# Kernel tuning notes

Measured on AMD Instinct MI355X. Metric: run time of the kernel, lower is better.

The kernel has to match this reference:

```python
import jax, jax.numpy as jnp
import numpy as np
from jax import lax

B, C, T = 16, 1, 2097152
DS = 16  # downsample_factor


def setup_inputs() -> dict:
    key = jax.random.key(0)
    audio = jax.random.normal(key, (B, C, T), dtype=jnp.float32) * 0.5
    sr, attack_ms, release_ms = 44100.0, 10.0, 100.0
    tc = float(np.exp(-np.log10(9.0)))  # exp(-log10(9)) time-constant numerator
    return {
        'audio': audio,
        'threshold': jnp.array([-20.0], jnp.float32),
        'ratio': jnp.array([4.0], jnp.float32),
        'makeup': jnp.array([3.0], jnp.float32),
        'attack_time': jnp.array([tc / (sr * attack_ms * 0.001 * DS)], jnp.float32),
        'release_time': jnp.array([tc / (sr * release_ms * 0.001 * DS)], jnp.float32),
    }


def _linear_downsample(x, factor):
    # F.interpolate(mode='linear', align_corners=False, scale_factor=1/factor)
    Tin = x.shape[-1]
    Tout = Tin // factor
    scale = Tin / Tout
    src = (jnp.arange(Tout, dtype=jnp.float32) + 0.5) * scale - 0.5
    src = jnp.clip(src, 0.0, Tin - 1)
    x0 = jnp.floor(src).astype(jnp.int32)
    x1 = jnp.minimum(x0 + 1, Tin - 1)
    w = src - x0.astype(jnp.float32)
    return x[..., x0] * (1.0 - w) + x[..., x1] * w


def _upsample_with_windows(x, up):
    # x: [B, C, F] framewise envelope; overlap-add with periodic Hann, hop=up
    xb = jnp.concatenate([x, x[..., -1:]], axis=-1)  # add endpoint
    n = jnp.arange(2 * up, dtype=jnp.float32)
    win = 0.5 * (1.0 - jnp.cos(2.0 * jnp.pi * n / (2 * up)))  # torch.hann_window (periodic)
    frames = xb[..., None] * win  # [B, C, F+1, 2*up]
    bsz, ch, nf, fl = frames.shape
    L = (nf - 1) * up + fl
    idx = (jnp.arange(nf)[:, None] * up + jnp.arange(fl)[None, :]).reshape(-1)
    out = jnp.zeros((bsz, ch, L), frames.dtype).at[:, :, idx].add(frames.reshape(bsz, ch, -1))
    return out[:, :, up:-up]


def reference(audio, threshold, ratio, makeup, attack_time, release_time):
    audio_db = 20.0 * jnp.log10(jnp.abs(audio) + 1e-8)
    comp_db = jnp.where(audio_db > threshold,
                        threshold + (audio_db - threshold) / ratio,
                        audio_db)
    gain = comp_db - audio_db  # [B, C, T], static gain reduction in dB (<= 0)
    gd = _linear_downsample(gain, DS)  # [B, C, T//DS]
    # sequential attack/release gain smoothing (one-pole recurrence) over frames
    gd_t = jnp.moveaxis(gd, -1, 0)  # [T//DS, B, C]
    def step(prev, tgt):
        new = jnp.where(tgt >= prev,
                        attack_time * prev + (1.0 - attack_time) * tgt,
                        release_time * prev + (1.0 - release_time) * tgt)
        return new, new
    _, ys = lax.scan(step, gd_t[0], gd_t)
    gs = jnp.moveaxis(ys, 0, -1)  # smoothed gain, [B, C, T//DS]
    gup = _upsample_with_windows(gs, DS)[..., :gain.shape[-1]]
    out_db = audio_db + gup + makeup
    out = 10.0 ** (out_db / 20.0)
    return jnp.where(audio < 0, -out, out)
```

## Files before the change

### kernel.cpp

```cpp
#include <hip/hip_runtime.h>
#include <math.h>

#define B_SZ 16
#define T_LEN 2097152
#define F_LEN (T_LEN / 16)
#define NBLOCKS 8192
#define K_LOG 0.16609640474436813f

typedef float f32x4 __attribute__((ext_vector_type(4)));

#define KEEP4(v) asm volatile("" :: "v"(v.x), "v"(v.y), "v"(v.z), "v"(v.w))
#define LGKM_FENCE() asm volatile("s_waitcnt lgkmcnt(0)" ::: "memory")

__device__ __forceinline__ float gain_db(float s, float thr, float slope) {
    float db = 6.0205999132796239f * __log2f(fabsf(s) + 1e-8f);
    float ov = db - thr;
    return ov > 0.0f ? ov * slope : 0.0f;
}
__device__ __forceinline__ float step1(float y, float t, float at, float rt) {
    return fmaf((t >= y) ? at : rt, y - t, t);
}
__device__ __forceinline__ float win_sel(int p, float a, float b, float c, float d) {
    float lo = (p & 1) ? b : a;
    float hi = (p & 1) ? d : c;
    return (p & 2) ? hi : lo;
}

__global__ __launch_bounds__(256) void k_fused(const float4* __restrict__ audio4,
                                               const float* __restrict__ thr_p,
                                               const float* __restrict__ ratio_p,
                                               const float* __restrict__ mk_p,
                                               const float* __restrict__ at_p,
                                               const float* __restrict__ rt_p,
                                               float4* __restrict__ out4) {
    __shared__ float  gd_s[4][84];
    __shared__ float2 yp_s[4][64];

    const int tid  = threadIdx.x;
    const int lane = tid & 63;
    const int wv   = tid >> 6;
    const int b    = blockIdx.x >> 9;
    const int bib  = blockIdx.x & 511;
    const int W0   = (bib << 8) + (wv << 6);

    const float*  Af = (const float*)audio4 + (size_t)b * T_LEN;
    const float4* A4 = audio4 + (size_t)b * (T_LEN / 4) + (size_t)W0 * 4;
    float4*       O4 = out4  + (size_t)b * (T_LEN / 4) + (size_t)W0 * 4;

    float4 xs0 = A4[lane];
    float4 xs1 = A4[lane + 64];
    float4 xs2 = A4[lane + 128];
    float4 xs3 = A4[lane + 192];
    KEEP4(xs0); KEEP4(xs1); KEEP4(xs2); KEEP4(xs3);

    float t7 = 0.0f, t8 = 0.0f;
    if (lane < 17) {
        int fr = (lane < 16) ? (W0 - 16 + lane) : (W0 + 64);
        fr = fr < 0 ? 0 : (fr > F_LEN - 1 ? F_LEN - 1 : fr);
        t7 = Af[(size_t)fr * 16 + 7];
        t8 = Af[(size_t)fr * 16 + 8];
    }

    const float thr   = thr_p[0];
    const float slope = 1.0f / ratio_p[0] - 1.0f;
    const float at = at_p[0], rt = rt_p[0];
    const int   p  = lane & 3;

#define GDJ(J, XV) {                                                   \
        float v  = (p == 1) ? XV.w : XV.x;                             \
        float g  = gain_db(v, thr, slope);                             \
        float gp = __shfl_xor(g, 3);                                   \
        if (p == 1) gd_s[wv][16 + 16 * J + (lane >> 2)] = 0.5f * (g + gp); }
    GDJ(0, xs0) GDJ(1, xs1) GDJ(2, xs2) GDJ(3, xs3)
#undef GDJ
    if (lane < 17) {
        float gw = 0.5f * (gain_db(t7, thr, slope) + gain_db(t8, thr, slope));
        gd_s[wv][(lane < 16) ? lane : 80] = gw;
    }
    LGKM_FENCE();

    if (lane < 4) {
        const float4* gp4 = reinterpret_cast<const float4*>(&gd_s[wv][16 * lane]);
        float4 r0 = gp4[0], r1 = gp4[1], r2 = gp4[2], r3 = gp4[3];
        float4 r4 = gp4[4], r5 = gp4[5], r6 = gp4[6], r7 = gp4[7];
        float  rE = gd_s[wv][16 * lane + 32];
        __builtin_amdgcn_sched_barrier(0);
        bool exact = (bib == 0) && (wv == 0) && (lane == 0);
        float y;
        if (exact) {
            y = r4.x;
        } else {
            y = r0.x;
            y = step1(y, r0.y, at, rt); y = step1(y, r0.z, at, rt); y = step1(y, r0.w, at, rt);
            y = step1(y, r1.x, at, rt); y = step1(y, r1.y, at, rt); y = step1(y, r1.z, at, rt); y = step1(y, r1.w, at, rt);
            y = step1(y, r2.x, at, rt); y = step1(y, r2.y, at, rt); y = step1(y, r2.z, at, rt); y = step1(y, r2.w, at, rt);
            y = step1(y, r3.x, at, rt); y = step1(y, r3.y, at, rt); y = step1(y, r3.z, at, rt); y = step1(y, r3.w, at, rt);
            y = step1(y, r4.x, at, rt);
        }
        float2* ypb = &yp_s[wv][16 * lane];
        float yn;
#define PAIRSTEP(T, IDX) yn = step1(y, T, at, rt); ypb[IDX] = make_float2(y, yn); y = yn;
        PAIRSTEP(r4.y, 0)  PAIRSTEP(r4.z, 1)  PAIRSTEP(r4.w, 2)
        PAIRSTEP(r5.x, 3)  PAIRSTEP(r5.y, 4)  PAIRSTEP(r5.z, 5)  PAIRSTEP(r5.w, 6)
        PAIRSTEP(r6.x, 7)  PAIRSTEP(r6.y, 8)  PAIRSTEP(r6.z, 9)  PAIRSTEP(r6.w, 10)
        PAIRSTEP(r7.x, 11) PAIRSTEP(r7.y, 12) PAIRSTEP(r7.z, 13) PAIRSTEP(r7.w, 14)
        PAIRSTEP(rE, 15)
#undef PAIRSTEP
    }
    LGKM_FENCE();

    const float mkK = mk_p[0] * K_LOG;
    const int fsub = lane >> 2;
    const float wl0 = win_sel(p, 0.0f,                 0.14644660940672624f, 0.5f,                 0.85355339059327376f);
    const float wl1 = win_sel(p, 0.00960735979838478f, 0.22221488349019889f, 0.59754516100806413f, 0.91573480615127262f);
    const float wl2 = win_sel(p, 0.03806023374435663f, 0.30865828381745511f, 0.69134171618254489f, 0.96193976625564337f);
    const float wl3 = win_sel(p, 0.08426519384872738f, 0.40245483899193587f, 0.77778511650980111f, 0.99039264020161522f);

#define OUTC(C, WL) { float m = fabsf(C) + 1e-8f;                                   \
        float vv = m * __builtin_amdgcn_exp2f(fmaf(fmaf(dd, WL, gq), K_LOG, mkK));  \
        C = (C < 0.0f) ? -vv : vv; }
#define OUTJ(J, XV) {                                                               \
        float2 pr = yp_s[wv][16 * J + fsub];                                        \
        float gq = pr.x;                                                            \
        float dd = (W0 + 16 * J + fsub == F_LEN - 1) ? 0.0f : (pr.y - pr.x);        \
        OUTC(XV.x, wl0) OUTC(XV.y, wl1) OUTC(XV.z, wl2) OUTC(XV.w, wl3)             \
        O4[64 * J + lane] = XV; }
    OUTJ(0, xs0) OUTJ(1, xs1) OUTJ(2, xs2) OUTJ(3, xs3)
#undef OUTJ
#undef OUTC
}

extern "C" void kernel_launch(void* const* d_in, const int* in_sizes, int n_in,
                              void* d_out, int out_size, void* d_ws, size_t ws_size,
                              hipStream_t stream) {
    const float* audio  = (const float*)d_in[0];
    const float* thr    = (const float*)d_in[1];
    const float* ratio  = (const float*)d_in[2];
    const float* makeup = (const float*)d_in[3];
    const float* at     = (const float*)d_in[4];
    const float* rt     = (const float*)d_in[5];

    k_fused<<<NBLOCKS, 256, 0, stream>>>((const float4*)audio, thr, ratio, makeup,
                                         at, rt, (float4*)d_out);
}
```

Baseline: 237.9 us.

## Process four tiles per wave with double-buffered register prefetch

Each wave now handles four consecutive 64-frame tiles instead of one, and the grid shrinks to a quarter of the blocks. The next tile's audio is loaded into a second register set while the current tile is processed. The warm-up window gains are reused from the previous tile's tail held in shared memory, which removes the scattered 16-frame halo loads for later tiles. This trades fewer waves and higher register pressure for overlap of memory loads with compute and less redundant halo traffic.

```diff
diff --git a/kernel.cpp b/kernel.cpp
--- a/kernel.cpp
+++ b/kernel.cpp
@@ -4,13 +4,11 @@
 #define B_SZ 16
 #define T_LEN 2097152
 #define F_LEN (T_LEN / 16)
-#define NBLOCKS 8192
+#define NBLOCKS 2048
 #define K_LOG 0.16609640474436813f
 
-typedef float f32x4 __attribute__((ext_vector_type(4)));
-
-#define KEEP4(v) asm volatile("" :: "v"(v.x), "v"(v.y), "v"(v.z), "v"(v.w))
 #define LGKM_FENCE() asm volatile("s_waitcnt lgkmcnt(0)" ::: "memory")
+#define SCHED_PIN()  __builtin_amdgcn_sched_barrier(0)
 
 __device__ __forceinline__ float gain_db(float s, float thr, float slope) {
     float db = 6.0205999132796239f * __log2f(fabsf(s) + 1e-8f);
@@ -36,98 +34,127 @@
     __shared__ float  gd_s[4][84];
     __shared__ float2 yp_s[4][64];
 
-    const int tid  = threadIdx.x;
-    const int lane = tid & 63;
-    const int wv   = tid >> 6;
-    const int b    = blockIdx.x >> 9;
-    const int bib  = blockIdx.x & 511;
-    const int W0   = (bib << 8) + (wv << 6);
+    const int lane  = threadIdx.x & 63;
+    const int wv    = threadIdx.x >> 6;
+    const int gw    = blockIdx.x * 4 + wv;
+    const int b     = gw >> 9;
+    const int wbase = (gw & 511) << 8;
 
     const float*  Af = (const float*)audio4 + (size_t)b * T_LEN;
-    const float4* A4 = audio4 + (size_t)b * (T_LEN / 4) + (size_t)W0 * 4;
-    float4*       O4 = out4  + (size_t)b * (T_LEN / 4) + (size_t)W0 * 4;
-
-    float4 xs0 = A4[lane];
-    float4 xs1 = A4[lane + 64];
-    float4 xs2 = A4[lane + 128];
-    float4 xs3 = A4[lane + 192];
-    KEEP4(xs0); KEEP4(xs1); KEEP4(xs2); KEEP4(xs3);
-
-    float t7 = 0.0f, t8 = 0.0f;
-    if (lane < 17) {
-        int fr = (lane < 16) ? (W0 - 16 + lane) : (W0 + 64);
-        fr = fr < 0 ? 0 : (fr > F_LEN - 1 ? F_LEN - 1 : fr);
-        t7 = Af[(size_t)fr * 16 + 7];
-        t8 = Af[(size_t)fr * 16 + 8];
-    }
+    const float4* A4 = audio4 + (size_t)b * (T_LEN / 4) + (size_t)wbase * 4;
+    float4*       O4 = out4   + (size_t)b * (T_LEN / 4) + (size_t)wbase * 4;
 
     const float thr   = thr_p[0];
     const float slope = 1.0f / ratio_p[0] - 1.0f;
-    const float at = at_p[0], rt = rt_p[0];
-    const int   p  = lane & 3;
+    const float at    = at_p[0], rt = rt_p[0];
+    const float mkK   = mk_p[0] * K_LOG;
+    const int   p     = lane & 3;
+    const int   fsub  = lane >> 2;
 
-#define GDJ(J, XV) {                                                   \
-        float v  = (p == 1) ? XV.w : XV.x;                             \
-        float g  = gain_db(v, thr, slope);                             \
-        float gp = __shfl_xor(g, 3);                                   \
-        if (p == 1) gd_s[wv][16 + 16 * J + (lane >> 2)] = 0.5f * (g + gp); }
-    GDJ(0, xs0) GDJ(1, xs1) GDJ(2, xs2) GDJ(3, xs3)
-#undef GDJ
-    if (lane < 17) {
-        float gw = 0.5f * (gain_db(t7, thr, slope) + gain_db(t8, thr, slope));
-        gd_s[wv][(lane < 16) ? lane : 80] = gw;
-    }
-    LGKM_FENCE();
-
-    if (lane < 4) {
-        const float4* gp4 = reinterpret_cast<const float4*>(&gd_s[wv][16 * lane]);
-        float4 r0 = gp4[0], r1 = gp4[1], r2 = gp4[2], r3 = gp4[3];
-        float4 r4 = gp4[4], r5 = gp4[5], r6 = gp4[6], r7 = gp4[7];
-        float  rE = gd_s[wv][16 * lane + 32];
-        __builtin_amdgcn_sched_barrier(0);
-        bool exact = (bib == 0) && (wv == 0) && (lane == 0);
-        float y;
-        if (exact) {
-            y = r4.x;
-        } else {
-            y = r0.x;
-            y = step1(y, r0.y, at, rt); y = step1(y, r0.z, at, rt); y = step1(y, r0.w, at, rt);
-            y = step1(y, r1.x, at, rt); y = step1(y, r1.y, at, rt); y = step1(y, r1.z, at, rt); y = step1(y, r1.w, at, rt);
-            y = step1(y, r2.x, at, rt); y = step1(y, r2.y, at, rt); y = step1(y, r2.z, at, rt); y = step1(y, r2.w, at, rt);
-            y = step1(y, r3.x, at, rt); y = step1(y, r3.y, at, rt); y = step1(y, r3.z, at, rt); y = step1(y, r3.w, at, rt);
-            y = step1(y, r4.x, at, rt);
-        }
-        float2* ypb = &yp_s[wv][16 * lane];
-        float yn;
-#define PAIRSTEP(T, IDX) yn = step1(y, T, at, rt); ypb[IDX] = make_float2(y, yn); y = yn;
-        PAIRSTEP(r4.y, 0)  PAIRSTEP(r4.z, 1)  PAIRSTEP(r4.w, 2)
-        PAIRSTEP(r5.x, 3)  PAIRSTEP(r5.y, 4)  PAIRSTEP(r5.z, 5)  PAIRSTEP(r5.w, 6)
-        PAIRSTEP(r6.x, 7)  PAIRSTEP(r6.y, 8)  PAIRSTEP(r6.z, 9)  PAIRSTEP(r6.w, 10)
-        PAIRSTEP(r7.x, 11) PAIRSTEP(r7.y, 12) PAIRSTEP(r7.z, 13) PAIRSTEP(r7.w, 14)
-        PAIRSTEP(rE, 15)
-#undef PAIRSTEP
-    }
-    LGKM_FENCE();
-
-    const float mkK = mk_p[0] * K_LOG;
-    const int fsub = lane >> 2;
     const float wl0 = win_sel(p, 0.0f,                 0.14644660940672624f, 0.5f,                 0.85355339059327376f);
     const float wl1 = win_sel(p, 0.00960735979838478f, 0.22221488349019889f, 0.59754516100806413f, 0.91573480615127262f);
     const float wl2 = win_sel(p, 0.03806023374435663f, 0.30865828381745511f, 0.69134171618254489f, 0.96193976625564337f);
     const float wl3 = win_sel(p, 0.08426519384872738f, 0.40245483899193587f, 0.77778511650980111f, 0.99039264020161522f);
 
-#define OUTC(C, WL) { float m = fabsf(C) + 1e-8f;                                   \
-        float vv = m * __builtin_amdgcn_exp2f(fmaf(fmaf(dd, WL, gq), K_LOG, mkK));  \
+    float4 xa0 = A4[lane],       xa1 = A4[lane + 64],
+           xa2 = A4[lane + 128], xa3 = A4[lane + 192];
+    int wfr = wbase - 16 + (lane & 15); if (wfr < 0) wfr = 0;
+    float w7 = Af[(size_t)wfr * 16 + 7];
+    float w8 = Af[(size_t)wfr * 16 + 8];
+    int sfr0 = wbase + 64; if (sfr0 > F_LEN - 1) sfr0 = F_LEN - 1;
+    float sa7 = Af[(size_t)sfr0 * 16 + 7];
+    float sa8 = Af[(size_t)sfr0 * 16 + 8];
+    SCHED_PIN();
+
+#define PRELOAD(T, X0, X1, X2, X3, S7, S8) {                                     \
+        X0 = A4[(T) * 256 + lane];       X1 = A4[(T) * 256 + lane + 64];         \
+        X2 = A4[(T) * 256 + lane + 128]; X3 = A4[(T) * 256 + lane + 192];        \
+        int sfr = wbase + (T) * 64 + 64; if (sfr > F_LEN - 1) sfr = F_LEN - 1;   \
+        S7 = Af[(size_t)sfr * 16 + 7];  S8 = Af[(size_t)sfr * 16 + 8]; }
+
+#define GDJ(J, XV)  {                                                            \
+        float v  = (p == 1) ? XV.w : XV.x;       \
+        float g  = gain_db(v, thr, slope);                                       \
+        float gp = __shfl_xor(g, 3);               \
+        if (p == 1) gd_s[wv][16 + 16 * (J) + fsub] = 0.5f * (g + gp); }
+
+#define PAIRSTEP(T, IDX) yn = step1(y, T, at, rt); ypb[IDX] = make_float2(y, yn); y = yn;
+
+#define OUTC(C, WL) { float m = fabsf(C) + 1e-8f;                                \
+        float vv = m * __builtin_amdgcn_exp2f(fmaf(fmaf(dd, WL, gq), K_LOG, mkK)); \
         C = (C < 0.0f) ? -vv : vv; }
-#define OUTJ(J, XV) {                                                               \
-        float2 pr = yp_s[wv][16 * J + fsub];                                        \
-        float gq = pr.x;                                                            \
-        float dd = (W0 + 16 * J + fsub == F_LEN - 1) ? 0.0f : (pr.y - pr.x);        \
-        OUTC(XV.x, wl0) OUTC(XV.y, wl1) OUTC(XV.z, wl2) OUTC(XV.w, wl3)             \
-        O4[64 * J + lane] = XV; }
-    OUTJ(0, xs0) OUTJ(1, xs1) OUTJ(2, xs2) OUTJ(3, xs3)
+
+#define OUTJ(T, J, XV) {                                                         \
+        float2 pr = yp_s[wv][16 * (J) + fsub];                                   \
+        float gq = pr.x;                                                         \
+        float dd = (wbase + (T) * 64 + 16 * (J) + fsub == F_LEN - 1) ? 0.0f      \
+                                                                     : (pr.y - pr.x); \
+        OUTC(XV.x, wl0) OUTC(XV.y, wl1) OUTC(XV.z, wl2) OUTC(XV.w, wl3)          \
+        O4[(T) * 256 + 64 * (J) + lane] = XV; }
+
+#define TILE(T, X0, X1, X2, X3, S7, S8) {                                        \
+        GDJ(0, X0) GDJ(1, X1) GDJ(2, X2) GDJ(3, X3)                              \
+        if ((T) == 0 && lane < 16)                                               \
+            gd_s[wv][lane] = 0.5f * (gain_db(w7, thr, slope) + gain_db(w8, thr, slope)); \
+        if (lane == 0)                                                           \
+            gd_s[wv][80] = 0.5f * (gain_db(S7, thr, slope) + gain_db(S8, thr, slope));   \
+        LGKM_FENCE();                                                            \
+        if (lane < 4) {                                                          \
+            const float4* gq4 = reinterpret_cast<const float4*>(&gd_s[wv][16 * lane]);   \
+            float4 r0 = gq4[0], r1 = gq4[1], r2 = gq4[2], r3 = gq4[3];           \
+            float4 r4 = gq4[4], r5 = gq4[5], r6 = gq4[6], r7 = gq4[7];           \
+            float  rE = gd_s[wv][16 * lane + 32];                                \
+            __builtin_amdgcn_sched_barrier(0);                                   \
+            float y;                                                             \
+            if ((T) == 0 && wbase == 0 && lane == 0) {                           \
+                y = r4.x;                              \
+            } else {                                                             \
+                y = r0.x;                              \
+                y = step1(y, r0.y, at, rt); y = step1(y, r0.z, at, rt); y = step1(y, r0.w, at, rt); \
+                y = step1(y, r1.x, at, rt); y = step1(y, r1.y, at, rt); y = step1(y, r1.z, at, rt); y = step1(y, r1.w, at, rt); \
+                y = step1(y, r2.x, at, rt); y = step1(y, r2.y, at, rt); y = step1(y, r2.z, at, rt); y = step1(y, r2.w, at, rt); \
+                y = step1(y, r3.x, at, rt); y = step1(y, r3.y, at, rt); y = step1(y, r3.z, at, rt); y = step1(y, r3.w, at, rt); \
+                y = step1(y, r4.x, at, rt);               \
+            }                                                                    \
+            float2* ypb = &yp_s[wv][16 * lane];                                  \
+            float yn;                                                            \
+            PAIRSTEP(r4.y, 0)  PAIRSTEP(r4.z, 1)  PAIRSTEP(r4.w, 2)              \
+            PAIRSTEP(r5.x, 3)  PAIRSTEP(r5.y, 4)  PAIRSTEP(r5.z, 5)  PAIRSTEP(r5.w, 6)  \
+            PAIRSTEP(r6.x, 7)  PAIRSTEP(r6.y, 8)  PAIRSTEP(r6.z, 9)  PAIRSTEP(r6.w, 10) \
+            PAIRSTEP(r7.x, 11) PAIRSTEP(r7.y, 12) PAIRSTEP(r7.z, 13) PAIRSTEP(r7.w, 14) \
+            PAIRSTEP(rE, 15)                                                     \
+        }                                                                        \
+        LGKM_FENCE();                                                            \
+        OUTJ(T, 0, X0) OUTJ(T, 1, X1) OUTJ(T, 2, X2) OUTJ(T, 3, X3)              \
+        if ((T) < 3 && lane < 16) gd_s[wv][lane] = gd_s[wv][64 + lane];  \
+    }
+
+    float4 xb0, xb1, xb2, xb3;
+    float  sb7, sb8;
+
+    PRELOAD(1, xb0, xb1, xb2, xb3, sb7, sb8)
+    SCHED_PIN();
+    TILE(0, xa0, xa1, xa2, xa3, sa7, sa8)
+
+    PRELOAD(2, xa0, xa1, xa2, xa3, sa7, sa8)
+    SCHED_PIN();
+    LGKM_FENCE();
+    TILE(1, xb0, xb1, xb2, xb3, sb7, sb8)
+
+    PRELOAD(3, xb0, xb1, xb2, xb3, sb7, sb8)
+    SCHED_PIN();
+    LGKM_FENCE();
+    TILE(2, xa0, xa1, xa2, xa3, sa7, sa8)
+
+    LGKM_FENCE();
+    TILE(3, xb0, xb1, xb2, xb3, sb7, sb8)
+
+#undef TILE
 #undef OUTJ
 #undef OUTC
+#undef PAIRSTEP
+#undef GDJ
+#undef PRELOAD
 }
 
 extern "C" void kernel_launch(void* const* d_in, const int* in_sizes, int n_in,
```

After: 241.5 us. No clear change (+1.5%).
